# Kernel optimization log

Measured on AMD Instinct MI355X. Metric: run time of the kernel, lower is better.

Reference implementation:

```python
import jax, jax.numpy as jnp
import numpy as np

N, VQ, VK, C, H = 4, 4096, 4096, 128, 64


def setup_inputs() -> dict:
    key = jax.random.key(0)
    kx, ky, kq, kk, kv = jax.random.split(key, 5)
    # xavier-uniform-ish scale for params
    def xavier(k, shape):
        fan_in, fan_out = shape
        lim = (6.0 / (fan_in + fan_out)) ** 0.5
        return jax.random.uniform(k, shape, jnp.float32, -lim, lim)
    return {
        "x": jax.random.normal(kx, (N, VQ, C), jnp.float32),
        "y": jax.random.normal(ky, (N, VK, C), jnp.float32),
        "Wq": xavier(kq, (C, H)),
        "Wk": xavier(kk, (C, H)),
        "Wv": xavier(kv, (C, C)),
    }


def reference(x, y, Wq, Wk, Wv):
    # x: [n, vq, c], y: [n, vk, c]
    scale = Wq.shape[1] ** (-0.5)
    q = jnp.einsum('nvc,co->nvo', x, Wq)   # [n, vq, h]
    k = jnp.einsum('nvc,co->nvo', y, Wk)   # [n, vk, h]
    v = jnp.einsum('nvc,co->nvo', y, Wv)   # [n, vk, c]
    scores = jnp.einsum('nqc,nkc->nqk', q, k) * scale  # [n, vq, vk]
    attn = jax.nn.softmax(scores, axis=-1)
    return jnp.einsum('nqk,nkc->nqc', attn, v)         # [n, vq, c]
```

## Files before the change

kernel.cpp:

```cpp
#include <hip/hip_runtime.h>

typedef __bf16 bf16x8 __attribute__((ext_vector_type(8)));
typedef __bf16 bf16x4 __attribute__((ext_vector_type(4)));
typedef __bf16 bf16x2 __attribute__((ext_vector_type(2)));
typedef float  f32x4  __attribute__((ext_vector_type(4)));
typedef float  f32x16 __attribute__((ext_vector_type(16)));
typedef int    i32x4  __attribute__((ext_vector_type(4)));

#define MFMA16 __builtin_amdgcn_mfma_f32_16x16x32_bf16
#define MFMA32 __builtin_amdgcn_mfma_f32_32x32x16_bf16

static constexpr int BATCH = 4;
static constexpr int SEQ   = 4096;
static constexpr int CDIM  = 128;
static constexpr int HDIM  = 64;
static constexpr float FIXMAX = 16.0f;

union FB2  { bf16x2 h; int i; };
union I4B8 { i32x4 i; bf16x8 b; };

__device__ inline bf16x8 load8f_cvt(const float* __restrict__ p) {
    f32x4 a = *reinterpret_cast<const f32x4*>(p);
    f32x4 b = *reinterpret_cast<const f32x4*>(p + 4);
    bf16x8 r;
    r[0] = (__bf16)a[0]; r[1] = (__bf16)a[1]; r[2] = (__bf16)a[2]; r[3] = (__bf16)a[3];
    r[4] = (__bf16)b[0]; r[5] = (__bf16)b[1]; r[6] = (__bf16)b[2]; r[7] = (__bf16)b[3];
    return r;
}


__global__ __launch_bounds__(256) void proj_all_kernel(
    const float* __restrict__ x, const float* __restrict__ y,
    const float* __restrict__ Wq, const float* __restrict__ Wk,
    const float* __restrict__ Wv,
    __bf16* __restrict__ Qw, __bf16* __restrict__ Kw, __bf16* __restrict__ Vtw,
    float qscale)
{
    __shared__ __bf16 Wt[64][136];
    __shared__ __bf16 Vtile[64][72];

    const int job = blockIdx.x >> 8;
    const int bx  = blockIdx.x & 255;
    const int t    = threadIdx.x;
    const int lane = t & 63;
    const int w    = t >> 6;
    const int m    = lane & 15;
    const int quad = lane >> 4;

    if (job <= 1) {
        const float* X    = job ? y  : x;
        const float* W    = job ? Wk : Wq;
        __bf16*      outp = job ? Kw : Qw;
        const float scale = job ? 1.0f : qscale;

        #pragma unroll
        for (int pass = 0; pass < 4; ++pass) {
            int flat = pass * 2048 + t * 8;
            int cin  = flat >> 6;
            int h0   = flat & 63;
            bf16x8 v = load8f_cvt(W + flat);
            #pragma unroll
            for (int j = 0; j < 8; ++j) Wt[h0 + j][cin] = v[j];
        }
        __syncthreads();

        const int row0 = bx * 64 + w * 16;
        bf16x8 af[4];
        #pragma unroll
        for (int kc = 0; kc < 4; ++kc)
            af[kc] = load8f_cvt(X + (long)(row0 + m) * 128 + kc * 32 + quad * 8);

        #pragma unroll
        for (int tn = 0; tn < 4; ++tn) {
            f32x4 acc = {0.f, 0.f, 0.f, 0.f};
            #pragma unroll
            for (int kc = 0; kc < 4; ++kc) {
                bf16x8 bfrag = *reinterpret_cast<const bf16x8*>(&Wt[tn * 16 + m][kc * 32 + quad * 8]);
                acc = MFMA16(af[kc], bfrag, acc, 0, 0, 0);
            }
            #pragma unroll
            for (int r = 0; r < 4; ++r) {
                int  kg   = row0 + quad * 4 + r;
                long addr = ((long)(kg >> 5) * 4 + tn) * 512
                          + ((m >> 3) * 32 + (kg & 31)) * 8 + (m & 7);
                outp[addr] = (__bf16)(acc[r] * scale);
            }
        }
    } else {
        const int cob = (job - 2) * 64;
        const int ct0 = (job - 2) * 2;

        #pragma unroll
        for (int pass = 0; pass < 4; ++pass) {
            int flat = pass * 2048 + t * 8;
            int cin  = flat >> 6;
            int co0  = flat & 63;
            bf16x8 v = load8f_cvt(Wv + cin * 128 + cob + co0);
            #pragma unroll
            for (int j = 0; j < 8; ++j) Wt[co0 + j][cin] = v[j];
        }
        __syncthreads();

        const int row0 = bx * 64 + w * 16;
        bf16x8 af[4];
        #pragma unroll
        for (int kc = 0; kc < 4; ++kc)
            af[kc] = load8f_cvt(y + (long)(row0 + m) * 128 + kc * 32 + quad * 8);

        #pragma unroll
        for (int tn = 0; tn < 4; ++tn) {
            f32x4 acc = {0.f, 0.f, 0.f, 0.f};
            #pragma unroll
            for (int kc = 0; kc < 4; ++kc) {
                bf16x8 bfrag = *reinterpret_cast<const bf16x8*>(&Wt[tn * 16 + m][kc * 32 + quad * 8]);
                acc = MFMA16(af[kc], bfrag, acc, 0, 0, 0);
            }
            bf16x4 pk;
            #pragma unroll
            for (int r = 0; r < 4; ++r) pk[r] = (__bf16)acc[r];
            *reinterpret_cast<bf16x4*>(&Vtile[tn * 16 + m][w * 16 + quad * 4]) = pk;
        }
        __syncthreads();

        #pragma unroll
        for (int pp = 0; pp < 2; ++pp) {
            int i       = pp * 256 + t;
            int c_local = i & 31;
            int hh      = (i >> 5) & 1;
            int kc2     = (i >> 6) & 1;
            int ct_l    = (i >> 7) & 1;
            int kt_l    = i >> 8;
            bf16x8 v = *reinterpret_cast<const bf16x8*>(
                &Vtile[ct_l * 32 + c_local][kt_l * 32 + kc2 * 16 + hh * 8]);
            long dst = ((long)(bx * 2 + kt_l) * 8 + (ct0 + ct_l) * 2 + kc2) * 512
                     + (hh * 32 + c_local) * 8;
            *reinterpret_cast<bf16x8*>(Vtw + dst) = v;
        }
    }
}

__global__ __launch_bounds__(1024, 4) void attn_kernel(
    const __bf16* __restrict__ Qs, const __bf16* __restrict__ Ks,
    const __bf16* __restrict__ Vs, float* __restrict__ out)
{
    __shared__ float mbuf[2][2][2][64][33];

    const int t    = threadIdx.x;
    const int lane = t & 63;
    const int w    = t >> 6;
    const int qs   = w & 1;
    const int ch   = (w >> 1) & 1;
    const int g    = w >> 2;
    const int qc   = lane & 31;
    const int h    = lane >> 5;

    const int bx  = blockIdx.x;
    const int n   = bx >> 6;
    const int qtl = bx & 63;

    const long QT = (long)n * 128 + qtl * 2 + qs;
    bf16x8 qf[4];
    #pragma unroll
    for (int kc = 0; kc < 4; ++kc)
        qf[kc] = *reinterpret_cast<const bf16x8*>(Qs + (QT * 4 + kc) * 512 + lane * 8);

    const __bf16* kb = Ks + ((long)n * 128 + g * 32) * 2048 + lane * 8;
    const __bf16* vb = Vs + ((long)n * 128 + g * 32) * 4096 + (long)ch * 4 * 512 + lane * 8;

    f32x16 o_acc[2];
    #pragma unroll
    for (int ctl = 0; ctl < 2; ++ctl)
        #pragma unroll
        for (int i = 0; i < 16; ++i) o_acc[ctl][i] = 0.f;
    float l_a = 0.f, l_b = 0.f;

    for (int kt = 0; kt < 32; ++kt) {
        bf16x8 kf[4], vf[4];
        const __bf16* kp = kb + (long)kt * 2048;
        const __bf16* vp = vb + (long)kt * 4096;
        #pragma unroll
        for (int kc = 0; kc < 4; ++kc)
            kf[kc] = *reinterpret_cast<const bf16x8*>(kp + kc * 512);
        #pragma unroll
        for (int j = 0; j < 4; ++j)
            vf[j] = *reinterpret_cast<const bf16x8*>(vp + j * 512);

        f32x16 s;
        #pragma unroll
        for (int i = 0; i < 16; ++i) s[i] = -FIXMAX;
        #pragma unroll
        for (int kc = 0; kc < 4; ++kc)
            s = MFMA32(kf[kc], qf[kc], s, 0, 0, 0);

        int Dw[8];
        #pragma unroll
        for (int r2 = 0; r2 < 8; ++r2) {
            float p0 = __builtin_amdgcn_exp2f(s[2 * r2]);
            float p1 = __builtin_amdgcn_exp2f(s[2 * r2 + 1]);
            l_a += p0; l_b += p1;
            FB2 u; u.h[0] = (__bf16)p0; u.h[1] = (__bf16)p1;
            Dw[r2] = u.i;
        }

        #pragma unroll
        for (int kc2 = 0; kc2 < 2; ++kc2) {
            int a0 = Dw[4 * kc2 + 0], a1 = Dw[4 * kc2 + 1];
            int a2 = Dw[4 * kc2 + 2], a3 = Dw[4 * kc2 + 3];
            int r0 = __shfl_xor(a0, 32, 64);
            int r1 = __shfl_xor(a1, 32, 64);
            int r2 = __shfl_xor(a2, 32, 64);
            int r3 = __shfl_xor(a3, 32, 64);
            I4B8 pb;
            pb.i[0] = h ? r2 : a0;
            pb.i[1] = h ? r3 : a1;
            pb.i[2] = h ? a2 : r0;
            pb.i[3] = h ? a3 : r1;
            #pragma unroll
            for (int ctl = 0; ctl < 2; ++ctl)
                o_acc[ctl] = MFMA32(vf[ctl * 2 + kc2], pb.b, o_acc[ctl], 0, 0, 0);
        }
    }

    float l_run = l_a + l_b;

    if (g >= 2) {
        float* dst = &mbuf[qs][ch][g - 2][lane][0];
        #pragma unroll
        for (int ctl = 0; ctl < 2; ++ctl)
            #pragma unroll
            for (int i = 0; i < 16; ++i) dst[ctl * 16 + i] = o_acc[ctl][i];
        dst[32] = l_run;
    }
    __syncthreads();
    if (g < 2) {
        const float* src = &mbuf[qs][ch][g][lane][0];
        #pragma unroll
        for (int ctl = 0; ctl < 2; ++ctl)
            #pragma unroll
            for (int i = 0; i < 16; ++i) o_acc[ctl][i] += src[ctl * 16 + i];
        l_run += src[32];
    }
    __syncthreads();
    if (g == 1) {
        float* dst = &mbuf[qs][ch][0][lane][0];
        #pragma unroll
        for (int ctl = 0; ctl < 2; ++ctl)
            #pragma unroll
            for (int i = 0; i < 16; ++i) dst[ctl * 16 + i] = o_acc[ctl][i];
        dst[32] = l_run;
    }
    __syncthreads();

    if (g == 0) {
        const float* src = &mbuf[qs][ch][0][lane][0];
        #pragma unroll
        for (int ctl = 0; ctl < 2; ++ctl)
            #pragma unroll
            for (int i = 0; i < 16; ++i) o_acc[ctl][i] += src[ctl * 16 + i];
        l_run += src[32];

        l_run += __shfl_xor(l_run, 32, 64);
        const float inv = 1.0f / l_run;
        const long row = (long)n * SEQ + qtl * 64 + qs * 32 + qc;
        #pragma unroll
        for (int ctl = 0; ctl < 2; ++ctl)
            #pragma unroll
            for (int rg = 0; rg < 4; ++rg) {
                f32x4 o;
                #pragma unroll
                for (int i = 0; i < 4; ++i) o[i] = o_acc[ctl][rg * 4 + i] * inv;
                *reinterpret_cast<f32x4*>(
                    out + row * CDIM + ch * 64 + ctl * 32 + rg * 8 + h * 4) = o;
            }
    }
}

extern "C" void kernel_launch(void* const* d_in, const int* in_sizes, int n_in,
                              void* d_out, int out_size, void* d_ws, size_t ws_size,
                              hipStream_t stream)
{
    const float* x  = (const float*)d_in[0];
    const float* y  = (const float*)d_in[1];
    const float* Wq = (const float*)d_in[2];
    const float* Wk = (const float*)d_in[3];
    const float* Wv = (const float*)d_in[4];
    float* out = (float*)d_out;

    __bf16* Qw  = (__bf16*)d_ws;
    __bf16* Kw  = Qw + (long)BATCH * SEQ * HDIM;
    __bf16* Vtw = Kw + (long)BATCH * SEQ * HDIM;

    const float qscale = 0.125f * 1.4426950408889634f;

    proj_all_kernel<<<dim3(1024), dim3(256), 0, stream>>>(
        x, y, Wq, Wk, Wv, Qw, Kw, Vtw, qscale);

    attn_kernel<<<dim3(256), dim3(1024), 0, stream>>>(Qw, Kw, Vtw, out);
}
```

Measured before the change: 120.0 us.

## Process both query subtiles per wave and double-buffer K/V register loads

```diff
diff --git a/kernel.cpp b/kernel.cpp
--- a/kernel.cpp
+++ b/kernel.cpp
@@ -139,7 +139,54 @@
     }
 }
 
-__global__ __launch_bounds__(1024, 4) void attn_kernel(
+__device__ __forceinline__ void softmax_pv(
+    const f32x16& s, const bf16x8 (&vf)[4], f32x16& o0, f32x16& o1,
+    float& l, int h)
+{
+    int Dw[8];
+    #pragma unroll
+    for (int r2 = 0; r2 < 8; ++r2) {
+        float p0 = __builtin_amdgcn_exp2f(s[2 * r2]);
+        float p1 = __builtin_amdgcn_exp2f(s[2 * r2 + 1]);
+        l += p0 + p1;
+        FB2 u; u.h[0] = (__bf16)p0; u.h[1] = (__bf16)p1;
+        Dw[r2] = u.i;
+    }
+    #pragma unroll
+    for (int kc2 = 0; kc2 < 2; ++kc2) {
+        int a0 = Dw[4 * kc2 + 0], a1 = Dw[4 * kc2 + 1];
+        int a2 = Dw[4 * kc2 + 2], a3 = Dw[4 * kc2 + 3];
+        int r0 = __shfl_xor(a0, 32, 64);
+        int r1 = __shfl_xor(a1, 32, 64);
+        int r2 = __shfl_xor(a2, 32, 64);
+        int r3 = __shfl_xor(a3, 32, 64);
+        I4B8 pb;
+        pb.i[0] = h ? r2 : a0;
+        pb.i[1] = h ? r3 : a1;
+        pb.i[2] = h ? a2 : r0;
+        pb.i[3] = h ? a3 : r1;
+        o0 = MFMA32(vf[0 * 2 + kc2], pb.b, o0, 0, 0, 0);
+        o1 = MFMA32(vf[1 * 2 + kc2], pb.b, o1, 0, 0, 0);
+    }
+}
+
+__device__ __forceinline__ void attn_step(
+    const bf16x8 (&kf)[4], const bf16x8 (&vf)[4], const bf16x8 (&qf)[2][4],
+    f32x16 (&o_acc)[4], float (&l)[2], int h)
+{
+    f32x16 s0, s1;
+    #pragma unroll
+    for (int i = 0; i < 16; ++i) { s0[i] = -FIXMAX; s1[i] = -FIXMAX; }
+    #pragma unroll
+    for (int kc = 0; kc < 4; ++kc) {
+        s0 = MFMA32(kf[kc], qf[0][kc], s0, 0, 0, 0);
+        s1 = MFMA32(kf[kc], qf[1][kc], s1, 0, 0, 0);
+    }
+    softmax_pv(s0, vf, o_acc[0], o_acc[1], l[0], h);
+    softmax_pv(s1, vf, o_acc[2], o_acc[3], l[1], h);
+}
+
+__global__ __launch_bounds__(512, 2) void attn_kernel(
     const __bf16* __restrict__ Qs, const __bf16* __restrict__ Ks,
     const __bf16* __restrict__ Vs, float* __restrict__ out)
 {
@@ -148,9 +195,8 @@
     const int t    = threadIdx.x;
     const int lane = t & 63;
     const int w    = t >> 6;
-    const int qs   = w & 1;
-    const int ch   = (w >> 1) & 1;
-    const int g    = w >> 2;
+    const int ch   = w & 1;
+    const int g    = w >> 1;
     const int qc   = lane & 31;
     const int h    = lane >> 5;
 
@@ -158,120 +204,120 @@
     const int n   = bx >> 6;
     const int qtl = bx & 63;
 
-    const long QT = (long)n * 128 + qtl * 2 + qs;
-    bf16x8 qf[4];
+    bf16x8 qf[2][4];
+    #pragma unroll
+    for (int st = 0; st < 2; ++st) {
+        const long QT = (long)n * 128 + qtl * 2 + st;
+        #pragma unroll
+        for (int kc = 0; kc < 4; ++kc)
+            qf[st][kc] = *reinterpret_cast<const bf16x8*>(Qs + (QT * 4 + kc) * 512 + lane * 8);
+    }
+
+    const __bf16* kb = Ks + ((long)n * 128 + g * 32) * 2048 + lane * 8;
+    const __bf16* vb = Vs + ((long)n * 128 + g * 32) * 4096 + (long)ch * 2048 + lane * 8;
+
+    f32x16 o_acc[4];
+    #pragma unroll
+    for (int a = 0; a < 4; ++a)
+        #pragma unroll
+        for (int i = 0; i < 16; ++i) o_acc[a][i] = 0.f;
+    float l[2] = {0.f, 0.f};
+
+    bf16x8 kfA[4], vfA[4], kfB[4], vfB[4];
+
     #pragma unroll
     for (int kc = 0; kc < 4; ++kc)
-        qf[kc] = *reinterpret_cast<const bf16x8*>(Qs + (QT * 4 + kc) * 512 + lane * 8);
-
-    const __bf16* kb = Ks + ((long)n * 128 + g * 32) * 2048 + lane * 8;
-    const __bf16* vb = Vs + ((long)n * 128 + g * 32) * 4096 + (long)ch * 4 * 512 + lane * 8;
-
-    f32x16 o_acc[2];
-    #pragma unroll
-    for (int ctl = 0; ctl < 2; ++ctl)
-        #pragma unroll
-        for (int i = 0; i < 16; ++i) o_acc[ctl][i] = 0.f;
-    float l_a = 0.f, l_b = 0.f;
-
-    for (int kt = 0; kt < 32; ++kt) {
-        bf16x8 kf[4], vf[4];
-        const __bf16* kp = kb + (long)kt * 2048;
-        const __bf16* vp = vb + (long)kt * 4096;
-        #pragma unroll
-        for (int kc = 0; kc < 4; ++kc)
-            kf[kc] = *reinterpret_cast<const bf16x8*>(kp + kc * 512);
-        #pragma unroll
-        for (int j = 0; j < 4; ++j)
-            vf[j] = *reinterpret_cast<const bf16x8*>(vp + j * 512);
-
-        f32x16 s;
-        #pragma unroll
-        for (int i = 0; i < 16; ++i) s[i] = -FIXMAX;
-        #pragma unroll
-        for (int kc = 0; kc < 4; ++kc)
-            s = MFMA32(kf[kc], qf[kc], s, 0, 0, 0);
-
-        int Dw[8];
-        #pragma unroll
-        for (int r2 = 0; r2 < 8; ++r2) {
-            float p0 = __builtin_amdgcn_exp2f(s[2 * r2]);
-            float p1 = __builtin_amdgcn_exp2f(s[2 * r2 + 1]);
-            l_a += p0; l_b += p1;
-            FB2 u; u.h[0] = (__bf16)p0; u.h[1] = (__bf16)p1;
-            Dw[r2] = u.i;
-        }
-
-        #pragma unroll
-        for (int kc2 = 0; kc2 < 2; ++kc2) {
-            int a0 = Dw[4 * kc2 + 0], a1 = Dw[4 * kc2 + 1];
-            int a2 = Dw[4 * kc2 + 2], a3 = Dw[4 * kc2 + 3];
-            int r0 = __shfl_xor(a0, 32, 64);
-            int r1 = __shfl_xor(a1, 32, 64);
-            int r2 = __shfl_xor(a2, 32, 64);
-            int r3 = __shfl_xor(a3, 32, 64);
-            I4B8 pb;
-            pb.i[0] = h ? r2 : a0;
-            pb.i[1] = h ? r3 : a1;
-            pb.i[2] = h ? a2 : r0;
-            pb.i[3] = h ? a3 : r1;
-            #pragma unroll
-            for (int ctl = 0; ctl < 2; ++ctl)
-                o_acc[ctl] = MFMA32(vf[ctl * 2 + kc2], pb.b, o_acc[ctl], 0, 0, 0);
-        }
-    }
-
-    float l_run = l_a + l_b;
+        kfA[kc] = *reinterpret_cast<const bf16x8*>(kb + kc * 512);
+    #pragma unroll
+    for (int j = 0; j < 4; ++j)
+        vfA[j] = *reinterpret_cast<const bf16x8*>(vb + j * 512);
+
+    for (int kt = 0; kt < 32; kt += 2) {
+        {
+            const __bf16* kp = kb + (long)(kt + 1) * 2048;
+            const __bf16* vp = vb + (long)(kt + 1) * 4096;
+            #pragma unroll
+            for (int kc = 0; kc < 4; ++kc)
+                kfB[kc] = *reinterpret_cast<const bf16x8*>(kp + kc * 512);
+            #pragma unroll
+            for (int j = 0; j < 4; ++j)
+                vfB[j] = *reinterpret_cast<const bf16x8*>(vp + j * 512);
+        }
+        attn_step(kfA, vfA, qf, o_acc, l, h);
+
+        if (kt < 30) {
+            const __bf16* kp = kb + (long)(kt + 2) * 2048;
+            const __bf16* vp = vb + (long)(kt + 2) * 4096;
+            #pragma unroll
+            for (int kc = 0; kc < 4; ++kc)
+                kfA[kc] = *reinterpret_cast<const bf16x8*>(kp + kc * 512);
+            #pragma unroll
+            for (int j = 0; j < 4; ++j)
+                vfA[j] = *reinterpret_cast<const bf16x8*>(vp + j * 512);
+        }
+        attn_step(kfB, vfB, qf, o_acc, l, h);
+    }
 
     if (g >= 2) {
-        float* dst = &mbuf[qs][ch][g - 2][lane][0];
-        #pragma unroll
-        for (int ctl = 0; ctl < 2; ++ctl)
-            #pragma unroll
-            for (int i = 0; i < 16; ++i) dst[ctl * 16 + i] = o_acc[ctl][i];
-        dst[32] = l_run;
+        #pragma unroll
+        for (int st = 0; st < 2; ++st) {
+            float* dst = &mbuf[st][ch][g - 2][lane][0];
+            #pragma unroll
+            for (int ctl = 0; ctl < 2; ++ctl)
+                #pragma unroll
+                for (int i = 0; i < 16; ++i) dst[ctl * 16 + i] = o_acc[st * 2 + ctl][i];
+            dst[32] = l[st];
+        }
     }
     __syncthreads();
     if (g < 2) {
-        const float* src = &mbuf[qs][ch][g][lane][0];
-        #pragma unroll
-        for (int ctl = 0; ctl < 2; ++ctl)
-            #pragma unroll
-            for (int i = 0; i < 16; ++i) o_acc[ctl][i] += src[ctl * 16 + i];
-        l_run += src[32];
+        #pragma unroll
+        for (int st = 0; st < 2; ++st) {
+            const float* src = &mbuf[st][ch][g][lane][0];
+            #pragma unroll
+            for (int ctl = 0; ctl < 2; ++ctl)
+                #pragma unroll
+                for (int i = 0; i < 16; ++i) o_acc[st * 2 + ctl][i] += src[ctl * 16 + i];
+            l[st] += src[32];
+        }
     }
     __syncthreads();
     if (g == 1) {
-        float* dst = &mbuf[qs][ch][0][lane][0];
-        #pragma unroll
-        for (int ctl = 0; ctl < 2; ++ctl)
-            #pragma unroll
-            for (int i = 0; i < 16; ++i) dst[ctl * 16 + i] = o_acc[ctl][i];
-        dst[32] = l_run;
+        #pragma unroll
+        for (int st = 0; st < 2; ++st) {
+            float* dst = &mbuf[st][ch][0][lane][0];
+            #pragma unroll
+            for (int ctl = 0; ctl < 2; ++ctl)
+                #pragma unroll
+                for (int i = 0; i < 16; ++i) dst[ctl * 16 + i] = o_acc[st * 2 + ctl][i];
+            dst[32] = l[st];
+        }
     }
     __syncthreads();
 
     if (g == 0) {
-        const float* src = &mbuf[qs][ch][0][lane][0];
-        #pragma unroll
-        for (int ctl = 0; ctl < 2; ++ctl)
-            #pragma unroll
-            for (int i = 0; i < 16; ++i) o_acc[ctl][i] += src[ctl * 16 + i];
-        l_run += src[32];
-
-        l_run += __shfl_xor(l_run, 32, 64);
-        const float inv = 1.0f / l_run;
-        const long row = (long)n * SEQ + qtl * 64 + qs * 32 + qc;
-        #pragma unroll
-        for (int ctl = 0; ctl < 2; ++ctl)
-            #pragma unroll
-            for (int rg = 0; rg < 4; ++rg) {
-                f32x4 o;
-                #pragma unroll
-                for (int i = 0; i < 4; ++i) o[i] = o_acc[ctl][rg * 4 + i] * inv;
-                *reinterpret_cast<f32x4*>(
-                    out + row * CDIM + ch * 64 + ctl * 32 + rg * 8 + h * 4) = o;
-            }
+        #pragma unroll
+        for (int st = 0; st < 2; ++st) {
+            const float* src = &mbuf[st][ch][0][lane][0];
+            #pragma unroll
+            for (int ctl = 0; ctl < 2; ++ctl)
+                #pragma unroll
+                for (int i = 0; i < 16; ++i) o_acc[st * 2 + ctl][i] += src[ctl * 16 + i];
+            float lr = l[st] + src[32];
+            lr += __shfl_xor(lr, 32, 64);
+            const float inv = 1.0f / lr;
+            const long row = (long)n * SEQ + qtl * 64 + st * 32 + qc;
+            #pragma unroll
+            for (int ctl = 0; ctl < 2; ++ctl)
+                #pragma unroll
+                for (int rg = 0; rg < 4; ++rg) {
+                    f32x4 o;
+                    #pragma unroll
+                    for (int i = 0; i < 4; ++i) o[i] = o_acc[st * 2 + ctl][rg * 4 + i] * inv;
+                    *reinterpret_cast<f32x4*>(
+                        out + row * CDIM + ch * 64 + ctl * 32 + rg * 8 + h * 4) = o;
+                }
+        }
     }
 }
 
@@ -295,5 +341,5 @@
     proj_all_kernel<<<dim3(1024), dim3(256), 0, stream>>>(
         x, y, Wq, Wk, Wv, Qw, Kw, Vtw, qscale);
 
-    attn_kernel<<<dim3(256), dim3(1024), 0, stream>>>(Qw, Kw, Vtw, out);
-}
+    attn_kernel<<<dim3(256), dim3(512), 0, stream>>>(Qw, Kw, Vtw, out);
+}
```

New measurement: 115.1 us. -4.1%, faster.
